# Kernel tuning notes

Measured on AMD Instinct MI355X. Metric: run time of the kernel, lower is better.

The kernel has to match this reference:

```python
import jax, jax.numpy as jnp
from jax import lax
import numpy as np

B, T, H, W = 8, 32, 128, 128
D_MODEL, D_STATE, D_CONV, EXPAND = 256, 16, 4, 2
D_INNER = EXPAND * D_MODEL
DT_RANK = 16  # ceil(d_model/16)
CHANS = [3, 32, 64, 96]
COV_SCALE = 0.01


def setup_inputs() -> dict:
    key = jax.random.key(0)
    ks = iter(jax.random.split(key, 64))
    def n(shape, s=0.02):
        return jax.random.normal(next(ks), shape, dtype=jnp.float32) * s
    inp = {
        "frames": jax.random.normal(next(ks), (B, T, 3, H, W), dtype=jnp.float32),
        "target_bboxes": jax.random.uniform(next(ks), (B, T, 4), dtype=jnp.float32),
    }
    for i in range(3):
        inp[f"conv_w{i}"] = n((CHANS[i + 1], CHANS[i], 3, 3, 3))
        inp[f"conv_b{i}"] = jnp.zeros((CHANS[i + 1],), jnp.float32)
        inp[f"bn_g{i}"] = jnp.ones((CHANS[i + 1],), jnp.float32)
        inp[f"bn_b{i}"] = jnp.zeros((CHANS[i + 1],), jnp.float32)
    inp["ep_w"] = n((D_MODEL, CHANS[-1])); inp["ep_b"] = jnp.zeros((D_MODEL,), jnp.float32)
    inp["bp1_w"] = n((64, 4), 0.1); inp["bp1_b"] = jnp.zeros((64,), jnp.float32)
    inp["bp2_w"] = n((D_MODEL, 64)); inp["bp2_b"] = jnp.zeros((D_MODEL,), jnp.float32)
    inp["in_proj_w"] = n((2 * D_INNER, D_MODEL))
    inp["conv1d_w"] = n((D_INNER, 1, D_CONV), 0.1)
    inp["conv1d_b"] = jnp.zeros((D_INNER,), jnp.float32)
    inp["x_proj_w"] = n((DT_RANK + 2 * D_STATE, D_INNER))
    inp["dt_proj_w"] = n((D_INNER, DT_RANK), 0.1)
    inp["dt_proj_b"] = jnp.full((D_INNER,), -3.0, jnp.float32)
    inp["A_log"] = jnp.log(jnp.broadcast_to(jnp.arange(1, D_STATE + 1, dtype=jnp.float32), (D_INNER, D_STATE)))
    inp["D_param"] = jnp.ones((D_INNER,), jnp.float32)
    inp["out_proj_w"] = n((D_MODEL, D_INNER))
    inp["h1_w"] = n((D_MODEL // 2, D_MODEL)); inp["h1_b"] = jnp.zeros((D_MODEL // 2,), jnp.float32)
    inp["h2_w"] = n((4, D_MODEL // 2), 0.1); inp["h2_b"] = jnp.zeros((4,), jnp.float32)
    inp["kf_F"] = jnp.eye(4, dtype=jnp.float32) + n((4, 4), 0.01)
    inp["kf_H"] = jnp.eye(4, dtype=jnp.float32) + n((4, 4), 0.01)
    inp["kf_log_q"] = n((4,), 1.0) - 2.0
    inp["kf_log_r"] = n((4,), 1.0) - 2.0
    return inp


DN3D = ("NCDHW", "OIDHW", "NCDHW")


def _forward(frames, target_bboxes, conv_w0, conv_b0, bn_g0, bn_b0,
             conv_w1, conv_b1, bn_g1, bn_b1, conv_w2, conv_b2, bn_g2, bn_b2,
             ep_w, ep_b, bp1_w, bp1_b, bp2_w, bp2_b,
             in_proj_w, conv1d_w, conv1d_b, x_proj_w, dt_proj_w, dt_proj_b,
             A_log, D_param, out_proj_w, h1_w, h1_b, h2_w, h2_b,
             kf_F, kf_H, kf_log_q, kf_log_r):
    Bn, Tn = frames.shape[0], frames.shape[1]

    # ---- bbox_proj: Linear(4,64) -> ReLU -> Linear(64,d_model) ----
    bf = jax.nn.relu(target_bboxes @ bp1_w.T + bp1_b) @ bp2_w.T + bp2_b  # (B,T,Dm)

    # ---- 3D conv encoder (BN in eval mode: running stats 0/1 -> affine only) ----
    x = jnp.transpose(frames, (0, 2, 1, 3, 4))  # (B,C,T,H,W)
    for (w, b, g, be) in ((conv_w0, conv_b0, bn_g0, bn_b0),
                          (conv_w1, conv_b1, bn_g1, bn_b1),
                          (conv_w2, conv_b2, bn_g2, bn_b2)):
        x = lax.conv_general_dilated(x, w, (1, 2, 2), ((1, 1), (1, 1), (1, 1)),
                                     dimension_numbers=DN3D) + b[None, :, None, None, None]
        x = g[None, :, None, None, None] * x + be[None, :, None, None, None]
        x = jax.nn.relu(x)
        x = lax.reduce_window(x, -jnp.inf, lax.max, (1, 1, 1, 2, 2), (1, 1, 1, 2, 2), "VALID")
    x = x.mean(axis=(3, 4))                    # AdaptiveAvgPool3d((None,1,1)) -> (B,Cenc,T)
    ff = jnp.transpose(x, (0, 2, 1)) @ ep_w.T + ep_b  # (B,T,Dm)

    u = ff + bf

    # ---- Mamba block ----
    xz = u @ in_proj_w.T                        # (B,T,2*Di)
    xm, z = jnp.split(xz, 2, axis=-1)
    xc = jnp.transpose(xm, (0, 2, 1))           # (B,Di,T)
    xc = lax.conv_general_dilated(xc, conv1d_w, (1,), ((D_CONV - 1, 0),),
                                  dimension_numbers=("NCW", "OIW", "NCW"),
                                  feature_group_count=D_INNER) + conv1d_b[None, :, None]
    xs = jax.nn.silu(jnp.transpose(xc, (0, 2, 1)))  # (B,T,Di)
    xdbl = xs @ x_proj_w.T
    dt, Bm, Cm = jnp.split(xdbl, [DT_RANK, DT_RANK + D_STATE], axis=-1)
    dt = jax.nn.softplus(dt @ dt_proj_w.T + dt_proj_b)    # (B,T,Di)
    A = -jnp.exp(A_log)                                    # (Di,Ds)
    dA = jnp.exp(dt[..., None] * A)                        # (B,T,Di,Ds)
    dBx = dt[..., None] * Bm[:, :, None, :] * xs[..., None]

    def ssm_step(h, inputs):
        dA_t, dBx_t, C_t = inputs
        h = dA_t * h + dBx_t                               # (B,Di,Ds)
        y = jnp.einsum("bds,bs->bd", h, C_t)
        return h, y

    h0 = jnp.zeros((Bn, D_INNER, D_STATE), xs.dtype)
    _, ys = lax.scan(ssm_step, h0, (jnp.transpose(dA, (1, 0, 2, 3)),
                                    jnp.transpose(dBx, (1, 0, 2, 3)),
                                    jnp.transpose(Cm, (1, 0, 2))))
    y = jnp.transpose(ys, (1, 0, 2)) + D_param * xs
    y = y * jax.nn.silu(z)
    mo = y @ out_proj_w.T                                  # (B,T,Dm)

    # ---- measurement head ----
    meas = jax.nn.sigmoid(jax.nn.relu(mo @ h1_w.T + h1_b) @ h2_w.T + h2_b)  # (B,T,4)

    # ---- Kalman filter over T (scan) ----
    Q = jnp.diag(jnp.exp(kf_log_q) + 1e-6)
    R = jnp.diag(jnp.exp(kf_log_r) + 1e-6)
    I4 = jnp.eye(4, dtype=meas.dtype)
    Hb = jnp.broadcast_to(kf_H, (Bn, 4, 4))

    def kf_step(carry, m_t):
        s, P = carry
        s_pred = jnp.einsum("ij,bjk->bik", kf_F, s)
        P_pred = jnp.einsum("ij,bjk,lk->bil", kf_F, P, kf_F) + Q
        yres = m_t - jnp.einsum("ij,bjk->bik", kf_H, s_pred)
        S = jnp.einsum("ij,bjk,lk->bil", kf_H, P_pred, kf_H) + R
        SinvH = jnp.linalg.solve(S, Hb)                    # S^{-1} H
        K = jnp.einsum("bij,bkj->bik", P_pred, SinvH)      # P H^T S^{-T}
        s_new = s_pred + K @ yres
        IKH = I4 - K @ kf_H
        P_new = IKH @ P_pred @ jnp.swapaxes(IKH, -1, -2) + (K @ R) @ jnp.swapaxes(K, -1, -2)
        return (s_new, P_new), s_new[..., 0]

    state0 = target_bboxes[:, 0, :, None]                  # (B,4,1)
    cov0 = jnp.broadcast_to(I4 * COV_SCALE, (Bn, 4, 4))
    _, preds = lax.scan(kf_step, (state0, cov0), jnp.transpose(meas, (1, 0, 2))[..., None])
    kf_pred = jnp.transpose(preds, (1, 0, 2))              # (B,T,4)
    return kf_pred, meas


def reference(frames, target_bboxes, conv_w0, conv_b0, bn_g0, bn_b0,
              conv_w1, conv_b1, bn_g1, bn_b1, conv_w2, conv_b2, bn_g2, bn_b2,
              ep_w, ep_b, bp1_w, bp1_b, bp2_w, bp2_b,
              in_proj_w, conv1d_w, conv1d_b, x_proj_w, dt_proj_w, dt_proj_b,
              A_log, D_param, out_proj_w, h1_w, h1_b, h2_w, h2_b,
              kf_F, kf_H, kf_log_q, kf_log_r):
    return _forward(frames, target_bboxes, conv_w0, conv_b0, bn_g0, bn_b0,
                    conv_w1, conv_b1, bn_g1, bn_b1, conv_w2, conv_b2, bn_g2, bn_b2,
                    ep_w, ep_b, bp1_w, bp1_b, bp2_w, bp2_b,
                    in_proj_w, conv1d_w, conv1d_b, x_proj_w, dt_proj_w, dt_proj_b,
                    A_log, D_param, out_proj_w, h1_w, h1_b, h2_w, h2_b,
                    kf_F, kf_H, kf_log_q, kf_log_r)
```

## Files before the change

kernel.cpp:

```cpp
#include <hip/hip_runtime.h>
#include <math.h>

constexpr int Bn = 8, Tn = 32;
constexpr int D_INNER = 512;

typedef __attribute__((ext_vector_type(8))) short short8;
typedef __attribute__((ext_vector_type(8))) unsigned short ushort8;
typedef __attribute__((ext_vector_type(4))) float f32x4;

__device__ inline unsigned short f2bf(float x) {
    unsigned int u = __float_as_uint(x);
    unsigned int r = (u + 0x7FFF + ((u >> 16) & 1)) >> 16;
    return (unsigned short)r;
}

__device__ __forceinline__ float kf_mm(float Av, float Bv, int i, int j, int gb) {
    float c = 0.f;
    #pragma unroll
    for (int k = 0; k < 4; ++k)
        c = fmaf(__shfl(Av, gb + i * 4 + k, 64), __shfl(Bv, gb + k * 4 + j, 64), c);
    return c;
}
__device__ __forceinline__ float kf_mmT(float Av, float Bv, int i, int j, int gb) {
    float c = 0.f;
    #pragma unroll
    for (int k = 0; k < 4; ++k)
        c = fmaf(__shfl(Av, gb + i * 4 + k, 64), __shfl(Bv, gb + j * 4 + k, 64), c);
    return c;
}

__global__ void prep_all(
    const float* __restrict__ cw0, const float* __restrict__ cw1,
    const float* __restrict__ cw2,
    const float* __restrict__ ip, const float* __restrict__ xp,
    const float* __restrict__ dt, const float* __restrict__ op,
    const float* __restrict__ h1, const float* __restrict__ h2,
    const float* __restrict__ ep, const float* __restrict__ bp2,
    const float* __restrict__ bp1,
    const float* __restrict__ kfF, const float* __restrict__ kfH,
    const float* __restrict__ lq, const float* __restrict__ lr,
    unsigned short* __restrict__ w0b, unsigned short* __restrict__ w1b,
    unsigned short* __restrict__ w2b, float* __restrict__ tW,
    float* __restrict__ kfK)
{
    int idx = blockIdx.x * blockDim.x + threadIdx.x;
    if (idx < 9216) {
        int d = idx;
        int sl = d & 7, sq = (d >> 3) & 3, co = (d >> 5) & 31;
        int r = d >> 10; int ky = r % 3, kt = r / 3;
        int q = sq ^ (co & 3) ^ ((co >> 2) & 3);
        float v = 0.f;
        if (q < 3 && sl < 3)
            v = cw0[((((size_t)co * 3 + sl) * 3 + kt) * 3 + ky) * 3 + q];
        w0b[d] = f2bf(v);
    } else if (idx < 64512) {
        int d = idx - 9216;
        int sl = d & 7, sg = (d >> 3) & 3, co = (d >> 5) & 63;
        int r = d >> 11; int k9 = r % 9, kt = r / 9;
        int ci = (sg ^ (co & 3)) * 8 + sl;
        w1b[d] = f2bf(cw1[((size_t)(co * 32 + ci) * 3 + kt) * 9 + k9]);
    } else if (idx < 230400) {
        int d = idx - 64512;
        int cip = d & 31; int rest = d >> 5;
        int co = rest % 96; rest /= 96;
        int k9 = rest % 9; int hh = rest / 9;
        int h = hh & 1, kt = hh >> 1;
        int ci = h * 32 + cip;
        w2b[d] = f2bf(cw2[((size_t)(co * 64 + ci) * 3 + kt) * 9 + k9]);
    } else if (idx < 730880) {
        int d = idx - 230400;
        if (d < 262144)      { int o = d >> 8, k = d & 255;
                               tW[k * 1024 + o] = ip[d]; }
        else if (d < 286720) { int s = d - 262144; int o = s >> 9, k = s & 511;
                               tW[262144 + k * 48 + o] = xp[s]; }
        else if (d < 294912) { int s = d - 286720; int o = s >> 4, k = s & 15;
                               tW[286720 + k * 512 + o] = dt[s]; }
        else if (d < 425984) { int s = d - 294912; int o = s >> 9, k = s & 511;
                               tW[294912 + k * 256 + o] = op[s]; }
        else if (d < 458752) { int s = d - 425984; int o = s >> 8, k = s & 255;
                               tW[425984 + k * 128 + o] = h1[s]; }
        else if (d < 459264) { int s = d - 458752; int o = s >> 7, k = s & 127;
                               tW[458752 + k * 4 + o] = h2[s]; }
        else if (d < 483840) { int s = d - 459264; int o = s / 96, k = s - o * 96;
                               tW[459264 + k * 256 + o] = ep[s]; }
        else if (d < 500224) { int s = d - 483840; int o = s >> 6, k = s & 63;
                               tW[483840 + k * 256 + o] = bp2[s]; }
        else                 { int s = d - 500224; int o = s >> 2, k = s & 3;
                               tW[500224 + k * 64 + o] = bp1[s]; }
    } else {
        if (threadIdx.x >= 64) return;
        int l16 = threadIdx.x & 15;
        int i = l16 >> 2, j = l16 & 3;
        int gb = threadIdx.x & 48;
        float Fv = kfF[l16], Hv = kfH[l16];
        float R4[4];
        #pragma unroll
        for (int k = 0; k < 4; ++k) R4[k] = expf(lr[k]) + 1e-6f;
        float qi = expf(lq[i]) + 1e-6f;
        float Pv = (i == j) ? 0.01f : 0.f;
        for (int t = 0; t < Tn; ++t) {
            float FPv = kf_mm(Fv, Pv, i, j, gb);
            float Ppv = kf_mmT(FPv, Fv, i, j, gb) + ((i == j) ? qi : 0.f);
            float HPv = kf_mm(Hv, Ppv, i, j, gb);
            float Sv = kf_mmT(HPv, Hv, i, j, gb) + ((i == j) ? R4[i] : 0.f);
            float Xv = Hv;
            #pragma unroll
            for (int c = 0; c < 4; ++c) {
                float piv = __shfl(Sv, gb + c * 5, 64);
                float dinv = 1.f / piv;
                if (i == c) { Sv *= dinv; Xv *= dinv; }
                float Scj = __shfl(Sv, gb + c * 4 + j, 64);
                float Xcj = __shfl(Xv, gb + c * 4 + j, 64);
                float f = __shfl(Sv, gb + i * 4 + c, 64);
                if (i != c) { Sv = fmaf(-f, Scj, Sv); Xv = fmaf(-f, Xcj, Xv); }
            }
            float Kv = kf_mmT(Ppv, Xv, i, j, gb);
            if (threadIdx.x < 16) kfK[t * 16 + l16] = Kv;
            float IKHv = ((i == j) ? 1.f : 0.f) - kf_mm(Kv, Hv, i, j, gb);
            float T1v = kf_mm(IKHv, Ppv, i, j, gb);
            float krk = 0.f;
            #pragma unroll
            for (int k = 0; k < 4; ++k)
                krk = fmaf(__shfl(Kv, gb + i * 4 + k, 64) * R4[k],
                           __shfl(Kv, gb + j * 4 + k, 64), krk);
            Pv = kf_mmT(T1v, IKHv, i, j, gb) + krk;
        }
    }
}

constexpr int C0_STR  = 68;
constexpr int C0_BLKS = 17 * C0_STR;

__global__ __launch_bounds__(512) void conv0_kernel(
    const float* __restrict__ in, const unsigned short* __restrict__ w0b,
    const float* __restrict__ bias, const float* __restrict__ gam,
    const float* __restrict__ bet, unsigned short* __restrict__ out)
{
    int tid  = threadIdx.x;
    int lane = tid & 63;
    int wv   = __builtin_amdgcn_readfirstlane(tid >> 6);
    int q    = lane >> 4;
    int l15  = lane & 15;
    int pyp  = wv >> 1;
    int hx   = wv & 1;
    int bI = blockIdx.x;
    int bt = bI >> 4, yt = (bI >> 1) & 7, xh = bI & 1;
    int b = bt >> 5, t = bt & 31;

    __shared__ __align__(16) unsigned short S[C0_BLKS * 8];
    __shared__ __align__(16) unsigned short W[9 * 32 * 32];

    f32x4 acc[2][2];
    #pragma unroll
    for (int dy = 0; dy < 2; ++dy)
        #pragma unroll
        for (int nt = 0; nt < 2; ++nt) acc[dy][nt] = (f32x4)0.f;

    {
        const uint4* wsrc = (const uint4*)w0b;
        uint4* wdst = (uint4*)W;
        for (int e = tid; e < 1152; e += 512) wdst[e] = wsrc[e];
    }

    int oxl = hx * 16 + l15;

    int offs[3]; bool oksp[3];
    #pragma unroll
    for (int i = 0; i < 3; ++i) {
        int e = tid + 512 * i;
        int r = e / C0_STR, c = e - r * C0_STR;
        int gy = 16 * yt - 1 + r;
        int x  = 64 * xh + c - 1;
        bool act = (e < C0_BLKS);
        oksp[i] = act && gy >= 0 && gy < 128 && x >= 0 && x < 128;
        offs[i] = gy * 128 + x;
    }

    float biv[2] = {bias[l15], bias[l15 + 16]};
    float gv [2] = {gam [l15], gam [l15 + 16]};
    float bev[2] = {bet [l15], bet [l15 + 16]};

    float pf[3][3];
    auto ldG = [&](int ts) {
        bool tok = ((unsigned)ts < (unsigned)Tn);
        const float* base = in + (size_t)(b * Tn + (tok ? ts : 0)) * 49152;
        #pragma unroll
        for (int i = 0; i < 3; ++i) {
            bool ok = tok && oksp[i];
            const float* p = base + offs[i];
            pf[i][0] = ok ? p[0]     : 0.f;
            pf[i][1] = ok ? p[16384] : 0.f;
            pf[i][2] = ok ? p[32768] : 0.f;
        }
    };
    auto stS = [&]() {
        #pragma unroll
        for (int i = 0; i < 3; ++i) {
            if (i < 2 || tid < C0_BLKS - 1024) {
                unsigned w0_, w1_;
                asm("v_cvt_pk_bf16_f32 %0, %1, %2" : "=v"(w0_) : "v"(pf[i][0]), "v"(pf[i][1]));
                asm("v_cvt_pk_bf16_f32 %0, %1, %2" : "=v"(w1_) : "v"(pf[i][2]), "v"(0.f));
                uint4 pk; pk.x = w0_; pk.y = w1_; pk.z = 0u; pk.w = 0u;
                *(uint4*)(S + (size_t)(tid + 512 * i) * 8) = pk;
            }
        }
    };
    auto compute = [&](int kt) {
        #pragma unroll
        for (int ky = 0; ky < 3; ++ky) {
            short8 bfr[2];
            #pragma unroll
            for (int nt = 0; nt < 2; ++nt) {
                int co = nt * 16 + l15;
                int i16 = ((kt * 3 + ky) * 32 + co) * 4 +
                          (q ^ (co & 3) ^ ((co >> 2) & 3));
                bfr[nt] = *(const short8*)(W + (size_t)i16 * 8);
            }
            #pragma unroll
            for (int dy = 0; dy < 2; ++dy) {
                int r = 4 * pyp + 2 * dy + ky;
                short8 af = (short8)0;
                if (q < 3)
                    af = *(const short8*)(S + (size_t)(r * C0_STR + 2 * oxl + q) * 8);
                #pragma unroll
                for (int nt = 0; nt < 2; ++nt)
                    acc[dy][nt] = __builtin_amdgcn_mfma_f32_16x16x32_bf16(
                        af, bfr[nt], acc[dy][nt], 0, 0, 0);
            }
        }
    };

    ldG(t - 1);
    stS();
    ldG(t);
    __syncthreads();
    compute(0);
    __syncthreads();
    stS();
    ldG(t + 1);
    __syncthreads();
    compute(1);
    __syncthreads();
    stS();
    __syncthreads();
    compute(2);

    unsigned short* dst = out + (size_t)bt * 32768;
    #pragma unroll
    for (int nt = 0; nt < 2; ++nt) {
        int co = nt * 16 + l15;
        float bi = biv[nt], g = gv[nt], be = bev[nt];
        #pragma unroll
        for (int j = 0; j < 2; ++j) {
            float m0 = fmaxf(fmaf(g, acc[0][nt][2 * j]     + bi, be), 0.f);
            float m1 = fmaxf(fmaf(g, acc[0][nt][2 * j + 1] + bi, be), 0.f);
            float m2 = fmaxf(fmaf(g, acc[1][nt][2 * j]     + bi, be), 0.f);
            float m3 = fmaxf(fmaf(g, acc[1][nt][2 * j + 1] + bi, be), 0.f);
            float p = fmaxf(fmaxf(m0, m1), fmaxf(m2, m3));
            int pox = xh * 16 + hx * 8 + q * 2 + j;
            int poy = yt * 4 + pyp;
            dst[(poy * 32 + pox) * 32 + co] = f2bf(p);
        }
    }
}

__global__ __launch_bounds__(512) void conv1_kernel(
    const unsigned short* __restrict__ in, const unsigned short* __restrict__ w1b,
    const float* __restrict__ bias, const float* __restrict__ gam,
    const float* __restrict__ bet, unsigned short* __restrict__ out)
{
    int tid  = threadIdx.x;
    int lane = tid & 63;
    int wv   = tid >> 6;
    int q    = lane >> 4;
    int l15  = lane & 15;
    int oyp  = wv >> 1;
    int nh   = wv & 1;
    int bt = blockIdx.x >> 1, half = blockIdx.x & 1;
    int b = bt >> 5, t = bt & 31;

    __shared__ __align__(16) unsigned short S[17 * 34 * 32];
    __shared__ __align__(16) unsigned short W[9 * 64 * 32];

    f32x4 acc[2][2];
    #pragma unroll
    for (int mt = 0; mt < 2; ++mt)
        #pragma unroll
        for (int nt = 0; nt < 2; ++nt) acc[mt][nt] = (f32x4)0.f;

    int  soff[5]; bool sok[5]; bool sact[5];
    #pragma unroll
    for (int i = 0; i < 5; ++i) {
        int e = tid + 512 * i;
        bool act = e < 17 * 34 * 4;
        int sb = e & 3;
        int pos = e >> 2;
        int ys = pos / 34, xs = pos - ys * 34;
        int g = sb ^ ((xs >> 1) & 3);
        int y = 16 * half + ys - 1, x = xs - 1;
        sact[i] = act;
        sok[i]  = act && y >= 0 && x >= 0 && x < 32;
        soff[i] = (y * 32 + x) * 32 + g * 8;
    }

    for (int kt = 0; kt < 3; ++kt) {
        int ts = t + kt - 1;
        if (ts < 0 || ts >= Tn) continue;
        __syncthreads();
        const unsigned short* src = in + (size_t)(b * Tn + ts) * 32768;
        #pragma unroll
        for (int i = 0; i < 5; ++i) {
            if (sact[i]) {
                ushort8 v = (ushort8)0;
                if (sok[i]) v = *(const ushort8*)(src + soff[i]);
                *(ushort8*)(S + (size_t)(tid + 512 * i) * 8) = v;
            }
        }
        {
            const uint4* wsrc = (const uint4*)(w1b + kt * 18432);
            uint4* wdst = (uint4*)W;
            for (int e = tid; e < 2304; e += 512) wdst[e] = wsrc[e];
        }
        __syncthreads();

        for (int k9 = 0; k9 < 9; ++k9) {
            int ky = k9 / 3, kx = k9 - ky * 3;
            short8 bf[2];
            #pragma unroll
            for (int nt = 0; nt < 2; ++nt) {
                int co = nh * 32 + nt * 16 + l15;
                int blk = (k9 * 64 + co) * 4 + (q ^ (co & 3));
                bf[nt] = *(const short8*)(W + blk * 8);
            }
            short8 af[2];
            #pragma unroll
            for (int mt = 0; mt < 2; ++mt) {
                int oyl = 2 * oyp + mt;
                int ys = 2 * oyl + ky;
                int xs = 2 * l15 + kx;
                int blk = (ys * 34 + xs) * 4 + (q ^ ((xs >> 1) & 3));
                af[mt] = *(const short8*)(S + blk * 8);
            }
            #pragma unroll
            for (int mt = 0; mt < 2; ++mt)
                #pragma unroll
                for (int nt = 0; nt < 2; ++nt)
                    acc[mt][nt] = __builtin_amdgcn_mfma_f32_16x16x32_bf16(
                        af[mt], bf[nt], acc[mt][nt], 0, 0, 0);
        }
    }

    unsigned short* dst = out + (size_t)bt * 4096;
    #pragma unroll
    for (int nt = 0; nt < 2; ++nt) {
        int co = nh * 32 + nt * 16 + l15;
        float bi = bias[co], g = gam[co], be = bet[co];
        #pragma unroll
        for (int j = 0; j < 2; ++j) {
            float m0 = fmaxf(fmaf(g, acc[0][nt][2 * j]     + bi, be), 0.f);
            float m1 = fmaxf(fmaf(g, acc[0][nt][2 * j + 1] + bi, be), 0.f);
            float m2 = fmaxf(fmaf(g, acc[1][nt][2 * j]     + bi, be), 0.f);
            float m3 = fmaxf(fmaf(g, acc[1][nt][2 * j + 1] + bi, be), 0.f);
            float p = fmaxf(fmaxf(m0, m1), fmaxf(m2, m3));
            int px = 2 * q + j, py = half * 4 + oyp;
            dst[(py * 8 + px) * 64 + co] = f2bf(p);
        }
    }
}

__global__ __launch_bounds__(192) void conv2_kernel(
    const unsigned short* __restrict__ in, const unsigned short* __restrict__ w2b,
    const float* __restrict__ bias, const float* __restrict__ gam,
    const float* __restrict__ bet, float* __restrict__ out)
{
    int tid  = threadIdx.x;
    int lane = tid & 63;
    int wv   = tid >> 6;
    int q    = lane >> 4;
    int l15  = lane & 15;
    int bt = blockIdx.x >> 1, ch = blockIdx.x & 1;
    int b = bt >> 5, t = bt & 31;

    __shared__ __align__(16) unsigned short W[432 * 5 * 8];
    __shared__ __align__(16) unsigned short S[81 * 5 * 8];

    f32x4 acc = (f32x4)0.f;

    for (int kt = 0; kt < 3; ++kt) {
        int ts = t + kt - 1;
        if (ts < 0 || ts >= Tn) continue;
        for (int h = 0; h < 2; ++h) {
            __syncthreads();
            const unsigned short* wsrc = w2b + (size_t)((kt * 2 + h) * 9) * 96 * 32;
            for (int e = tid; e < 1728; e += 192) {
                int r48 = e >> 2, qq = e & 3;
                int k9 = r48 / 48, cr = r48 - k9 * 48;
                uint4 v = *(const uint4*)(wsrc + (k9 * 96 + ch * 48 + cr) * 32 + qq * 8);
                *(uint4*)(W + (r48 * 5 + qq) * 8) = v;
            }
            const unsigned short* src = in + (size_t)(b * Tn + ts) * 4096 + h * 32;
            for (int e = tid; e < 324; e += 192) {
                int cb = e & 3, p = e >> 2;
                int ys = p / 9, xs = p - ys * 9;
                int y = ys - 1, x = xs - 1;
                ushort8 v = (ushort8)0;
                if (y >= 0 && x >= 0 && y < 8 && x < 8)
                    v = *(const ushort8*)(src + ((y * 8 + x) * 64 + cb * 8));
                *(ushort8*)(S + (size_t)(p * 5 + cb) * 8) = v;
            }
            __syncthreads();

            int oy = l15 >> 2, ox = l15 & 3;
            #pragma unroll
            for (int k9 = 0; k9 < 9; ++k9) {
                int ky = k9 / 3, kx = k9 - ky * 3;
                short8 bf = *(const short8*)(W + (size_t)((k9 * 48 + wv * 16 + l15) * 5 + q) * 8);
                int p = (2 * oy + ky) * 9 + (2 * ox + kx);
                short8 af = *(const short8*)(S + (size_t)(p * 5 + q) * 8);
                acc = __builtin_amdgcn_mfma_f32_16x16x32_bf16(af, bf, acc, 0, 0, 0);
            }
        }
    }

    int co = ch * 48 + wv * 16 + l15;
    float bi = bias[co], g = gam[co], be = bet[co];
    float v0 = fmaxf(fmaf(g, acc[0] + bi, be), 0.f);
    float v1 = fmaxf(fmaf(g, acc[1] + bi, be), 0.f);
    float v2 = fmaxf(fmaf(g, acc[2] + bi, be), 0.f);
    float v3 = fmaxf(fmaf(g, acc[3] + bi, be), 0.f);
    float p0 = fmaxf(v0, v1);
    float p1 = fmaxf(v2, v3);
    float r0 = fmaxf(p0, __shfl_xor(p0, 16));
    float r1 = fmaxf(p1, __shfl_xor(p1, 16));
    if ((q & 1) == 0) {
        int py = q >> 1;
        float* o = out + (size_t)(bt * 96 + co) * 4 + py * 2;
        o[0] = r0;
        o[1] = r1;
    }
}

__global__ __launch_bounds__(256) void fuse_u_inproj(
    const float* __restrict__ buf2, const float* __restrict__ epT,
    const float* __restrict__ ep_b, const float* __restrict__ bb,
    const float* __restrict__ bp1T, const float* __restrict__ bp1_b,
    const float* __restrict__ bp2T, const float* __restrict__ bp2_b,
    const float* __restrict__ ipwT, float* __restrict__ xzb)
{
    int bt = blockIdx.x;
    int m  = threadIdx.x;
    __shared__ float hs[64];
    __shared__ float gap[96];
    __shared__ float u_lds[256];
    if (m < 64) {
        float a = bp1_b[m];
        #pragma unroll
        for (int k = 0; k < 4; ++k) a = fmaf(bp1T[k * 64 + m], bb[bt * 4 + k], a);
        hs[m] = fmaxf(a, 0.f);
    } else if (m < 160) {
        int c = m - 64;
        const float* p = buf2 + ((size_t)bt * 96 + c) * 4;
        gap[c] = 0.25f * (p[0] + p[1] + p[2] + p[3]);
    }
    __syncthreads();
    float ff = ep_b[m];
    for (int c = 0; c < 96; ++c) ff = fmaf(gap[c], epT[c * 256 + m], ff);
    float bfv = bp2_b[m];
    for (int j = 0; j < 64; ++j) bfv = fmaf(hs[j], bp2T[j * 256 + m], bfv);
    u_lds[m] = ff + bfv;
    __syncthreads();

    const float4* wbase = (const float4*)ipwT + m;
    float4 acc = {0.f, 0.f, 0.f, 0.f};
    for (int k = 0; k < 256; ++k) {
        float uk = u_lds[k];
        float4 w4 = wbase[(size_t)k * 256];
        acc.x = fmaf(uk, w4.x, acc.x);
        acc.y = fmaf(uk, w4.y, acc.y);
        acc.z = fmaf(uk, w4.z, acc.z);
        acc.w = fmaf(uk, w4.w, acc.w);
    }
    *(float4*)(xzb + (size_t)bt * 1024 + 4 * m) = acc;
}

__global__ __launch_bounds__(512) void convxd_kernel(
    const float* __restrict__ xzb, const float* __restrict__ c1w,
    const float* __restrict__ c1b, const float* __restrict__ xpw,
    const float* __restrict__ dtwT, const float* __restrict__ dt_b,
    float* __restrict__ xsb, float* __restrict__ xdb, float* __restrict__ dtbf)
{
    int bt = blockIdx.x;
    int b = bt >> 5, t = bt & 31;
    int tid = threadIdx.x;
    __shared__ float xs_lds[512];
    __shared__ float xd_lds[48];

    {
        float acc = c1b[tid];
        #pragma unroll
        for (int k = 0; k < 4; ++k) {
            int ts = t - 3 + k;
            if (ts >= 0)
                acc = fmaf(c1w[tid * 4 + k], xzb[(size_t)(b * Tn + ts) * 1024 + tid], acc);
        }
        float v = acc / (1.f + expf(-acc));
        xs_lds[tid] = v;
        xsb[(size_t)bt * 512 + tid] = v;
    }
    __syncthreads();

    {
        int wv = tid >> 6, ln = tid & 63;
        #pragma unroll
        for (int u = 0; u < 6; ++u) {
            int o = wv * 6 + u;
            const float* wrow = xpw + (size_t)o * 512;
            float acc = 0.f;
            #pragma unroll
            for (int e = 0; e < 8; ++e)
                acc = fmaf(wrow[ln + 64 * e], xs_lds[ln + 64 * e], acc);
            acc += __shfl_xor(acc, 32); acc += __shfl_xor(acc, 16);
            acc += __shfl_xor(acc, 8);  acc += __shfl_xor(acc, 4);
            acc += __shfl_xor(acc, 2);  acc += __shfl_xor(acc, 1);
            if (ln == 0) {
                xd_lds[o] = acc;
                xdb[(size_t)bt * 48 + o] = acc;
            }
        }
    }
    __syncthreads();

    {
        float a = dt_b[tid];
        #pragma unroll
        for (int k = 0; k < 16; ++k) a = fmaf(xd_lds[k], dtwT[k * 512 + tid], a);
        a = (a > 20.f) ? a : log1pf(expf(a));
        dtbf[(size_t)bt * 512 + tid] = a;
    }
}

__global__ __launch_bounds__(256) void ssm_kernel(
    const float* __restrict__ xdbl, const float* __restrict__ dtb,
    const float* __restrict__ xs, const float* __restrict__ xz,
    const float* __restrict__ A_log, const float* __restrict__ Dp,
    float* __restrict__ y)
{
    int tid = threadIdx.x;
    int lane = tid & 63;
    int s = lane & 15, dsub = lane >> 4;
    int gid = blockIdx.x * 4 + (tid >> 6);
    int b = gid >> 7;
    int d = ((gid & 127) << 2) + dsub;

    float A = -expf(A_log[d * 16 + s]);
    float Dv = Dp[d];
    float h = 0.f;
    for (int t = 0; t < Tn; ++t) {
        int bt = b * Tn + t;
        float dtv = dtb[(size_t)bt * 512 + d];
        float xv  = xs [(size_t)bt * 512 + d];
        float Bs  = xdbl[(size_t)bt * 48 + 16 + s];
        float Cs  = xdbl[(size_t)bt * 48 + 32 + s];
        float dA = expf(dtv * A);
        h = fmaf(dA, h, dtv * Bs * xv);
        float c = h * Cs;
        c += __shfl_xor(c, 8, 16);
        c += __shfl_xor(c, 4, 16);
        c += __shfl_xor(c, 2, 16);
        c += __shfl_xor(c, 1, 16);
        if (s == 0) {
            float zv = xz[(size_t)bt * 1024 + 512 + d];
            float sig = 1.f / (1.f + expf(-zv));
            y[(size_t)bt * 512 + d] = (c + Dv * xv) * (zv * sig);
        }
    }
}

__global__ __launch_bounds__(256) void out_head_kernel(
    const float* __restrict__ yb, const float* __restrict__ opwT,
    const float* __restrict__ h1wT, const float* __restrict__ h1_b,
    const float* __restrict__ h2w, const float* __restrict__ h2_b,
    float* __restrict__ meas_out)
{
    int bt = blockIdx.x;
    int m  = threadIdx.x;
    __shared__ float y_lds[512];
    __shared__ float mo_lds[256];
    __shared__ float hid_lds[128];

    y_lds[m]       = yb[(size_t)bt * 512 + m];
    y_lds[m + 256] = yb[(size_t)bt * 512 + m + 256];
    __syncthreads();

    {
        float a = 0.f;
        for (int k = 0; k < 512; ++k) a = fmaf(y_lds[k], opwT[k * 256 + m], a);
        mo_lds[m] = a;
    }
    __syncthreads();

    if (m < 128) {
        float a = h1_b[m];
        for (int k = 0; k < 256; ++k) a = fmaf(mo_lds[k], h1wT[k * 128 + m], a);
        hid_lds[m] = fmaxf(a, 0.f);
    }
    __syncthreads();

    if (m < 64) {
        int o2 = m >> 4, l15 = m & 15;
        float acc = 0.f;
        #pragma unroll
        for (int e = 0; e < 8; ++e)
            acc = fmaf(h2w[o2 * 128 + l15 + 16 * e], hid_lds[l15 + 16 * e], acc);
        acc += __shfl_xor(acc, 8, 16);
        acc += __shfl_xor(acc, 4, 16);
        acc += __shfl_xor(acc, 2, 16);
        acc += __shfl_xor(acc, 1, 16);
        if (l15 == 0) {
            float a = acc + h2_b[o2];
            meas_out[bt * 4 + o2] = 1.f / (1.f + expf(-a));
        }
    }
}

__global__ __launch_bounds__(128) void kf_kernel(
    const float* __restrict__ meas, const float* __restrict__ bb,
    const float* __restrict__ Fin, const float* __restrict__ Hmin,
    const float* __restrict__ kfK, float* __restrict__ pred)
{
    int tid = threadIdx.x;
    int b   = tid >> 4;
    int l16 = tid & 15;
    int i = l16 >> 2, j = l16 & 3;
    int gb = tid & 48;

    float Fv = Fin[l16], Hv = Hmin[l16];
    float sv = bb[b * 128 + j];

    for (int t = 0; t < Tn; ++t) {
        float mv = meas[(b * Tn + t) * 4 + j];
        float Kv = kfK[t * 16 + l16];
        float tr = Fv * sv;
        tr += __shfl_xor(tr, 1); tr += __shfl_xor(tr, 2);
        float spv = tr;
        float spj = __shfl(spv, gb + j * 4, 64);
        float hsp = Hv * spj;
        hsp += __shfl_xor(hsp, 1); hsp += __shfl_xor(hsp, 2);
        float yrv = mv - __shfl(hsp, gb + j * 4, 64);
        float t3 = Kv * yrv;
        t3 += __shfl_xor(t3, 1); t3 += __shfl_xor(t3, 2);
        float snv = spv + t3;
        if (j == 0) pred[(b * Tn + t) * 4 + i] = snv;
        sv = __shfl(snv, gb + j * 4, 64);
    }
}

extern "C" void kernel_launch(void* const* d_in, const int* in_sizes, int n_in,
                              void* d_out, int out_size, void* d_ws, size_t ws_size,
                              hipStream_t stream)
{
    const float* frames = (const float*)d_in[0];
    const float* bb     = (const float*)d_in[1];
    const float* cw0 = (const float*)d_in[2],  *cb0 = (const float*)d_in[3];
    const float* g0  = (const float*)d_in[4],  *be0 = (const float*)d_in[5];
    const float* cw1 = (const float*)d_in[6],  *cb1 = (const float*)d_in[7];
    const float* g1  = (const float*)d_in[8],  *be1 = (const float*)d_in[9];
    const float* cw2 = (const float*)d_in[10], *cb2 = (const float*)d_in[11];
    const float* g2  = (const float*)d_in[12], *be2 = (const float*)d_in[13];
    const float* ep_w  = (const float*)d_in[14], *ep_b  = (const float*)d_in[15];
    const float* bp1_w = (const float*)d_in[16], *bp1_b = (const float*)d_in[17];
    const float* bp2_w = (const float*)d_in[18], *bp2_b = (const float*)d_in[19];
    const float* in_proj_w = (const float*)d_in[20];
    const float* c1w = (const float*)d_in[21], *c1b = (const float*)d_in[22];
    const float* x_proj_w = (const float*)d_in[23];
    const float* dt_w = (const float*)d_in[24], *dt_b = (const float*)d_in[25];
    const float* A_log = (const float*)d_in[26], *Dp = (const float*)d_in[27];
    const float* out_proj_w = (const float*)d_in[28];
    const float* h1_w = (const float*)d_in[29], *h1_b = (const float*)d_in[30];
    const float* h2_w = (const float*)d_in[31], *h2_b = (const float*)d_in[32];
    const float* kfF = (const float*)d_in[33], *kfH = (const float*)d_in[34];
    const float* kfq = (const float*)d_in[35], *kfr = (const float*)d_in[36];

    float* ws   = (float*)d_ws;
    float* buf2 = ws;
    float* xzb  = buf2 + 98304;
    float* xsb  = xzb  + 262144;
    float* xdb  = xsb  + 131072;
    float* dtbf = xdb  + 12288;
    float* yb   = dtbf + 131072;
    float* tW   = yb   + 131072;
    float* kfK  = tW + 500480;
    unsigned short* buf0b = (unsigned short*)(kfK + 512);
    unsigned short* buf1b = buf0b + 8388608;
    unsigned short* w2b   = buf1b + 131072;
    unsigned short* w1b   = w2b + 165888;
    unsigned short* w0b   = w1b + 55296;

    float* ipwT = tW;
    float* dtwT = tW + 286720;
    float* opwT = tW + 294912;
    float* h1wT = tW + 425984;
    float* epwT = tW + 459264;
    float* bp2T = tW + 483840;
    float* bp1T = tW + 500224;

    float* kf_out   = (float*)d_out;
    float* meas_out = kf_out + Bn * Tn * 4;

    prep_all<<<dim3(2856), 256, 0, stream>>>(cw0, cw1, cw2,
                                             in_proj_w, x_proj_w, dt_w, out_proj_w,
                                             h1_w, h2_w, ep_w, bp2_w, bp1_w,
                                             kfF, kfH, kfq, kfr,
                                             w0b, w1b, w2b, tW, kfK);

    conv0_kernel<<<dim3(4096), 512, 0, stream>>>(frames, w0b, cb0, g0, be0, buf0b);
    conv1_kernel<<<dim3(512), 512, 0, stream>>>(buf0b, w1b, cb1, g1, be1, buf1b);
    conv2_kernel<<<dim3(512), 192, 0, stream>>>(buf1b, w2b, cb2, g2, be2, buf2);

    fuse_u_inproj<<<dim3(256), 256, 0, stream>>>(buf2, epwT, ep_b, bb, bp1T, bp1_b,
                                                 bp2T, bp2_b, ipwT, xzb);
    convxd_kernel<<<dim3(256), 512, 0, stream>>>(xzb, c1w, c1b, x_proj_w,
                                                 dtwT, dt_b, xsb, xdb, dtbf);
    ssm_kernel<<<dim3(256), 256, 0, stream>>>(xdb, dtbf, xsb, xzb, A_log, Dp, yb);
    out_head_kernel<<<dim3(256), 256, 0, stream>>>(yb, opwT, h1wT, h1_b,
                                                   h2_w, h2_b, meas_out);
    kf_kernel<<<dim3(1), 128, 0, stream>>>(meas_out, bb, kfF, kfH, kfK, kf_out);
}
```

Baseline: 322.5 us.

## Compute two output frames per conv0 block to reuse staged input slices

Each conv0 block now produces two consecutive time steps instead of one. It loads four input time slices in place of six, and each staged slice feeds the MFMA accumulators of both outputs that share it. The grid is halved to match. This cuts global loads, bf16 conversion and LDS staging of the frames by about a third, at the cost of twice the accumulator registers and fewer blocks in flight.

```diff
diff --git a/kernel.cpp b/kernel.cpp
--- a/kernel.cpp
+++ b/kernel.cpp
@@ -144,17 +144,20 @@
     int pyp  = wv >> 1;
     int hx   = wv & 1;
     int bI = blockIdx.x;
-    int bt = bI >> 4, yt = (bI >> 1) & 7, xh = bI & 1;
-    int b = bt >> 5, t = bt & 31;
+    int sp = bI & 15;
+    int yt = sp >> 1, xh = sp & 1;
+    int btc = bI >> 4;
+    int b = btc >> 4, tc = btc & 15;
+    int t0 = tc * 2;
 
     __shared__ __align__(16) unsigned short S[C0_BLKS * 8];
     __shared__ __align__(16) unsigned short W[9 * 32 * 32];
 
-    f32x4 acc[2][2];
+    f32x4 A0[2][2], A1[2][2];
     #pragma unroll
     for (int dy = 0; dy < 2; ++dy)
         #pragma unroll
-        for (int nt = 0; nt < 2; ++nt) acc[dy][nt] = (f32x4)0.f;
+        for (int nt = 0; nt < 2; ++nt) { A0[dy][nt] = (f32x4)0.f; A1[dy][nt] = (f32x4)0.f; }
 
     {
         const uint4* wsrc = (const uint4*)w0b;
@@ -205,63 +208,91 @@
             }
         }
     };
-    auto compute = [&](int kt) {
+    auto ldA = [&](int ky, short8 (&af)[2]) {
+        #pragma unroll
+        for (int dy = 0; dy < 2; ++dy) {
+            int r = 4 * pyp + 2 * dy + ky;
+            short8 a = (short8)0;
+            if (q < 3)
+                a = *(const short8*)(S + (size_t)(r * C0_STR + 2 * oxl + q) * 8);
+            af[dy] = a;
+        }
+    };
+    auto ldB = [&](int kt, int ky, short8 (&bf)[2]) {
+        #pragma unroll
+        for (int nt = 0; nt < 2; ++nt) {
+            int co = nt * 16 + l15;
+            int i16 = ((kt * 3 + ky) * 32 + co) * 4 +
+                      (q ^ (co & 3) ^ ((co >> 2) & 3));
+            bf[nt] = *(const short8*)(W + (size_t)i16 * 8);
+        }
+    };
+    auto mm = [&](short8 (&af)[2], short8 (&bf)[2], f32x4 (&A)[2][2]) {
+        #pragma unroll
+        for (int dy = 0; dy < 2; ++dy)
+            #pragma unroll
+            for (int nt = 0; nt < 2; ++nt)
+                A[dy][nt] = __builtin_amdgcn_mfma_f32_16x16x32_bf16(
+                    af[dy], bf[nt], A[dy][nt], 0, 0, 0);
+    };
+    auto cS1 = [&](int ktA, f32x4 (&A)[2][2]) {
         #pragma unroll
         for (int ky = 0; ky < 3; ++ky) {
-            short8 bfr[2];
-            #pragma unroll
-            for (int nt = 0; nt < 2; ++nt) {
-                int co = nt * 16 + l15;
-                int i16 = ((kt * 3 + ky) * 32 + co) * 4 +
-                          (q ^ (co & 3) ^ ((co >> 2) & 3));
-                bfr[nt] = *(const short8*)(W + (size_t)i16 * 8);
-            }
-            #pragma unroll
-            for (int dy = 0; dy < 2; ++dy) {
-                int r = 4 * pyp + 2 * dy + ky;
-                short8 af = (short8)0;
-                if (q < 3)
-                    af = *(const short8*)(S + (size_t)(r * C0_STR + 2 * oxl + q) * 8);
-                #pragma unroll
-                for (int nt = 0; nt < 2; ++nt)
-                    acc[dy][nt] = __builtin_amdgcn_mfma_f32_16x16x32_bf16(
-                        af, bfr[nt], acc[dy][nt], 0, 0, 0);
-            }
+            short8 af[2]; ldA(ky, af);
+            short8 bf[2];
+            ldB(ktA, ky, bf); mm(af, bf, A);
         }
     };
-
-    ldG(t - 1);
+    auto cS2 = [&](int ktA, f32x4 (&A)[2][2], int ktB, f32x4 (&B)[2][2]) {
+        #pragma unroll
+        for (int ky = 0; ky < 3; ++ky) {
+            short8 af[2]; ldA(ky, af);
+            short8 bf[2];
+            ldB(ktA, ky, bf); mm(af, bf, A);
+            ldB(ktB, ky, bf); mm(af, bf, B);
+        }
+    };
+    auto flush = [&](f32x4 (&A)[2][2], int t_out) {
+        unsigned short* dst = out + (size_t)(b * Tn + t_out) * 32768;
+        #pragma unroll
+        for (int nt = 0; nt < 2; ++nt) {
+            float bi = biv[nt], g = gv[nt], be = bev[nt];
+            int co = nt * 16 + l15;
+            #pragma unroll
+            for (int j = 0; j < 2; ++j) {
+                float m0 = fmaxf(fmaf(g, A[0][nt][2 * j]     + bi, be), 0.f);
+                float m1 = fmaxf(fmaf(g, A[0][nt][2 * j + 1] + bi, be), 0.f);
+                float m2 = fmaxf(fmaf(g, A[1][nt][2 * j]     + bi, be), 0.f);
+                float m3 = fmaxf(fmaf(g, A[1][nt][2 * j + 1] + bi, be), 0.f);
+                float p = fmaxf(fmaxf(m0, m1), fmaxf(m2, m3));
+                int pox = xh * 16 + hx * 8 + q * 2 + j;
+                int poy = yt * 4 + pyp;
+                dst[(poy * 32 + pox) * 32 + co] = f2bf(p);
+            }
+        }
+    };
+
+    ldG(t0 - 1);
     stS();
-    ldG(t);
-    __syncthreads();
-    compute(0);
+    ldG(t0);
+    __syncthreads();
+    cS1(0, A0);
     __syncthreads();
     stS();
-    ldG(t + 1);
-    __syncthreads();
-    compute(1);
+    ldG(t0 + 1);
+    __syncthreads();
+    cS2(1, A0, 0, A1);
     __syncthreads();
     stS();
-    __syncthreads();
-    compute(2);
-
-    unsigned short* dst = out + (size_t)bt * 32768;
-    #pragma unroll
-    for (int nt = 0; nt < 2; ++nt) {
-        int co = nt * 16 + l15;
-        float bi = biv[nt], g = gv[nt], be = bev[nt];
-        #pragma unroll
-        for (int j = 0; j < 2; ++j) {
-            float m0 = fmaxf(fmaf(g, acc[0][nt][2 * j]     + bi, be), 0.f);
-            float m1 = fmaxf(fmaf(g, acc[0][nt][2 * j + 1] + bi, be), 0.f);
-            float m2 = fmaxf(fmaf(g, acc[1][nt][2 * j]     + bi, be), 0.f);
-            float m3 = fmaxf(fmaf(g, acc[1][nt][2 * j + 1] + bi, be), 0.f);
-            float p = fmaxf(fmaxf(m0, m1), fmaxf(m2, m3));
-            int pox = xh * 16 + hx * 8 + q * 2 + j;
-            int poy = yt * 4 + pyp;
-            dst[(poy * 32 + pox) * 32 + co] = f2bf(p);
-        }
-    }
+    ldG(t0 + 2);
+    __syncthreads();
+    cS2(2, A0, 1, A1);
+    flush(A0, t0);
+    __syncthreads();
+    stS();
+    __syncthreads();
+    cS1(2, A1);
+    flush(A1, t0 + 1);
 }
 
 __global__ __launch_bounds__(512) void conv1_kernel(
@@ -713,7 +744,7 @@
                                              kfF, kfH, kfq, kfr,
                                              w0b, w1b, w2b, tW, kfK);
 
-    conv0_kernel<<<dim3(4096), 512, 0, stream>>>(frames, w0b, cb0, g0, be0, buf0b);
+    conv0_kernel<<<dim3(2048), 512, 0, stream>>>(frames, w0b, cb0, g0, be0, buf0b);
     conv1_kernel<<<dim3(512), 512, 0, stream>>>(buf0b, w1b, cb1, g1, be1, buf1b);
     conv2_kernel<<<dim3(512), 192, 0, stream>>>(buf1b, w2b, cb2, g2, be2, buf2);
 
```

After: 322.7 us. Within noise of the previous version (+0.1%).
